# Performance work log

Measured on AMD Instinct MI355X. Metric: run time of the kernel, lower is better.

## Reference

```python
import jax, jax.numpy as jnp
import numpy as np

B, S, E, H, ROT, MAXP = 2, 1024, 2048, 16, 64, 2048
HD = E // H
EPS = 1e-12  # torch F.normalize default eps


def _sinusoidal_positions(num_pos, dim):
    # GPT-J create_sinusoidal_positions: concat(sin, cos) along feature dim
    inv_freq = 1.0 / (10000.0 ** (np.arange(0, dim, 2, dtype=np.float32) / dim))
    sinusoid = np.einsum("i,j->ij", np.arange(num_pos, dtype=np.float32), inv_freq)
    return jnp.asarray(np.concatenate([np.sin(sinusoid), np.cos(sinusoid)], axis=-1))


def _rotate_every_two(x):
    x1 = x[..., ::2]
    x2 = x[..., 1::2]
    return jnp.stack((-x2, x1), axis=-1).reshape(x.shape)


def _apply_rotary(t, sin, cos):
    # t: [B,S,H,rot]; sin/cos: [B,S,rot/2] -> repeat_interleave(2) -> [B,S,1,rot]
    sin = jnp.repeat(sin, 2, axis=-1)[:, :, None, :]
    cos = jnp.repeat(cos, 2, axis=-1)[:, :, None, :]
    return t * cos + _rotate_every_two(t) * sin


def setup_inputs() -> dict:
    key = jax.random.key(0)
    ks = jax.random.split(key, 5)
    hidden_states = jax.random.normal(ks[0], (B, S, E), dtype=jnp.float32)
    w_q = jax.random.normal(ks[1], (E, E), dtype=jnp.float32) * 0.02
    w_k = jax.random.normal(ks[2], (E, E), dtype=jnp.float32) * 0.02
    w_v = jax.random.normal(ks[3], (E, E), dtype=jnp.float32) * 0.02
    w_o = jax.random.normal(ks[4], (E, E), dtype=jnp.float32) * 0.02
    norm_const = 0.5 * jnp.ones((1, H, 1, 1), dtype=jnp.float32)
    attention_mask = jnp.zeros((B, 1, 1, S), dtype=jnp.float32)  # 0 = attend (HF additive mask)
    position_ids = jnp.tile(jnp.arange(S, dtype=jnp.int32)[None, :], (B, 1))
    return {"hidden_states": hidden_states, "w_q": w_q, "w_k": w_k, "w_v": w_v,
            "w_o": w_o, "norm_const": norm_const, "attention_mask": attention_mask,
            "position_ids": position_ids}


def reference(hidden_states, w_q, w_k, w_v, w_o, norm_const, attention_mask, position_ids):
    b, s, e = hidden_states.shape
    # projections (nn.Linear, no bias): y = x @ W.T
    q = (hidden_states @ w_q.T).reshape(b, s, H, HD)  # rotary layout [B,S,H,hd]
    k = (hidden_states @ w_k.T).reshape(b, s, H, HD)
    v = (hidden_states @ w_v.T).reshape(b, s, H, HD).transpose(0, 2, 1, 3)  # [B,H,S,hd]

    embed = _sinusoidal_positions(MAXP, ROT)          # [MAXP, ROT]
    sincos = embed[position_ids]                      # [B,S,ROT]
    sin, cos = jnp.split(sincos, 2, axis=-1)          # each [B,S,ROT/2]

    # partial rotary on first ROT dims
    q = jnp.concatenate([_apply_rotary(q[..., :ROT], sin, cos), q[..., ROT:]], axis=-1)
    k = jnp.concatenate([_apply_rotary(k[..., :ROT], sin, cos), k[..., ROT:]], axis=-1)
    q = q.transpose(0, 2, 1, 3)  # [B,H,S,hd]
    k = k.transpose(0, 2, 1, 3)

    causal = jnp.tril(jnp.ones((s, s), dtype=bool))[None, None]   # [1,1,S,S]
    mask0 = (attention_mask == 0)                                  # [B,1,1,S] bool

    # value rescale: per-query count of visible keys ** sigmoid(norm_const), clamped >= 1
    counts = jnp.sum(causal & mask0, axis=-1, keepdims=True).astype(jnp.float32)  # [B,1,S,1]
    denom = jnp.maximum(counts ** jax.nn.sigmoid(norm_const), 1.0)                # [B,H,S,1]
    v = v / denom

    # L2-normalize q/k (torch F.normalize: x / max(||x||, eps))
    q = q / jnp.maximum(jnp.linalg.norm(q, axis=-1, keepdims=True), EPS)
    k = k / jnp.maximum(jnp.linalg.norm(k, axis=-1, keepdims=True), EPS)

    mask_t = jnp.swapaxes(mask0, -1, -2)  # [B,1,S,1]
    q = q * mask_t
    k = k * mask_t
    v = v * mask_t

    attn_weights = jnp.einsum("bhqd,bhkd->bhqk", q, k)     # cosine similarities
    attn_weights = jnp.where(causal, attn_weights, 0.0)
    attn_output = jnp.einsum("bhqk,bhkd->bhqd", attn_weights, v)

    attn_output = attn_output.transpose(0, 2, 1, 3).reshape(b, s, e)
    return attn_output @ w_o.T
```

## Files before the change

kernel.cpp:

```cpp
#include <hip/hip_runtime.h>
#include <math.h>

#define B 2
#define S 1024
#define E 2048
#define H 16
#define HD 128
#define ROT 64
#define EPSN 1e-12f

using half8 = __attribute__((ext_vector_type(8))) _Float16;
using half4 = __attribute__((ext_vector_type(4))) _Float16;
using half2 = __attribute__((ext_vector_type(2))) _Float16;
using f32x4 = __attribute__((ext_vector_type(4))) float;

__device__ __forceinline__ void gl_lds16(const void* g, void* l) {
    __builtin_amdgcn_global_load_lds(
        (const __attribute__((address_space(1))) unsigned int*)g,
        (__attribute__((address_space(3))) unsigned int*)l, 16, 0, 0);
}

#define BARX()   asm volatile("s_barrier" ::: "memory")
#define VMW(n)   asm volatile("s_waitcnt vmcnt(" #n ")" ::: "memory")
#define SCHEDB() __builtin_amdgcn_sched_barrier(0)

__device__ __forceinline__ int ctIdx(int row, int col) {
    return row * 256 + (col & 3) + ((((col >> 2) ^ ((row >> 3) & 15)) & 63) << 2);
}

__global__ __launch_bounds__(256) void f2h5(const float* __restrict__ x0,
                                            const float* __restrict__ x1,
                                            const float* __restrict__ x2,
                                            const float* __restrict__ x3,
                                            const float* __restrict__ x4,
                                            _Float16* __restrict__ y0,
                                            _Float16* __restrict__ y1,
                                            _Float16* __restrict__ y2,
                                            _Float16* __restrict__ y3,
                                            _Float16* __restrict__ y4) {
    const float* xs[5] = {x0, x1, x2, x3, x4};
    _Float16*    ys[5] = {y0, y1, y2, y3, y4};
    const int t = blockIdx.y;
    const int i = blockIdx.x * 256 + threadIdx.x;
    float4 v = ((const float4*)xs[t])[i];
    half4 h;
    h[0] = (_Float16)v.x; h[1] = (_Float16)v.y;
    h[2] = (_Float16)v.z; h[3] = (_Float16)v.w;
    ((half4*)ys[t])[i] = h;
}

__global__ __launch_bounds__(1024) void countprep(const float* __restrict__ am,
                                                  float* __restrict__ cnt) {
    __shared__ float sc[1024];
    const int b = blockIdx.x, t = threadIdx.x;
    sc[t] = (am[b * S + t] == 0.f) ? 1.f : 0.f;
    __syncthreads();
    for (int off = 1; off < 1024; off <<= 1) {
        float u = (t >= off) ? sc[t - off] : 0.f;
        __syncthreads();
        sc[t] += u;
        __syncthreads();
    }
    cnt[b * S + t] = sc[t];
}

__global__ __launch_bounds__(512, 2) void gemm_qkv256(
        const _Float16* __restrict__ hs,
        const _Float16* __restrict__ wq,
        const _Float16* __restrict__ wk,
        const _Float16* __restrict__ wv,
        _Float16* __restrict__ qo,
        _Float16* __restrict__ ko,
        _Float16* __restrict__ kto,
        _Float16* __restrict__ vto,
        const float* __restrict__ am,
        const int*  __restrict__ pos,
        const float* __restrict__ nc,
        const float* __restrict__ cnt) {
    __shared__ uint4 L[8][1024];
    __shared__ float sclA[256], sclB[256];

    const int lid = (int)blockIdx.x;
    const int swz = (lid & 7) * 24 + (lid >> 3);
    const int z   = swz >> 6;
    const int gm  = (swz & 63) >> 3;
    const int gn  = swz & 7;
    const _Float16* Wp = (z == 0) ? wq : (z == 1) ? wk : wv;
    const int mBase = gm << 8;
    const int nBase = gn << 8;

    const int tid   = (int)threadIdx.x;
    const int lane  = tid & 63;
    const int w     = tid >> 6;
    const int l15   = lane & 15;
    const int lq    = lane >> 4;
    const int wm4   = (w >> 2) << 2;
    const int wn2   = (w & 3) << 1;
    const int wbase = tid & 448;

    const int bb  = mBase >> 10;
    const int sB0 = mBase & (S - 1);
    const int h0  = gn * 2;

    if (tid < 256) {
        const int sgx = sB0 + tid;
        float valid = (am[bb * S + sgx] == 0.f) ? 1.f : 0.f;
        if (z == 2) {
            float c  = cnt[bb * S + sgx];
            float g0 = 1.f / (1.f + expf(-nc[h0]));
            float g1 = 1.f / (1.f + expf(-nc[h0 + 1]));
            sclA[tid] = valid / fmaxf(powf(c, g0), 1.f);
            sclB[tid] = valid / fmaxf(powf(c, g1), 1.f);
        } else {
            sclA[tid] = valid;
        }
    }

    f32x4 acc[2][2][4][2];
#pragma unroll
    for (int X = 0; X < 2; ++X)
#pragma unroll
        for (int Y = 0; Y < 2; ++Y)
#pragma unroll
            for (int mt = 0; mt < 4; ++mt)
#pragma unroll
                for (int nt = 0; nt < 2; ++nt)
                    acc[X][Y][mt][nt] = (f32x4){0.f, 0.f, 0.f, 0.f};

    half8 afA[4][2], afB[4][2], wfA[2][2], wfB[2][2];

    auto stage = [&](int slot, const _Float16* src, int rowBase, int hf, int kt) {
#pragma unroll
        for (int j = 0; j < 2; ++j) {
            const int c  = (j << 9) + tid;
            const int rb = c >> 7;
            const int q  = (c >> 4) & 7;
            const int r  = c & 15;
            gl_lds16(&src[(size_t)(rowBase + hf * 128 + rb * 16 + r) * E +
                          kt * 64 + q * 8],
                     &L[slot][(j << 9) + wbase]);
        }
    };
    auto ldsA = [&](half8 (&dst)[4][2], int slot) {
#pragma unroll
        for (int mt = 0; mt < 4; ++mt)
#pragma unroll
            for (int ks = 0; ks < 2; ++ks)
                dst[mt][ks] = *(const half8*)&L[slot]
                    [(wm4 + mt) * 128 + (ks * 4 + lq) * 16 + l15];
    };
    auto ldsB = [&](half8 (&dst)[2][2], int slot) {
#pragma unroll
        for (int nt = 0; nt < 2; ++nt)
#pragma unroll
            for (int ks = 0; ks < 2; ++ks)
                dst[nt][ks] = *(const half8*)&L[slot]
                    [(wn2 + nt) * 128 + (ks * 4 + lq) * 16 + l15];
    };

#define MMAQ(X, Y, Af, Bf)                                                     \
    do {                                                                       \
        __builtin_amdgcn_s_setprio(1);                                         \
        _Pragma("unroll") for (int mt = 0; mt < 4; ++mt)                       \
            _Pragma("unroll") for (int nt = 0; nt < 2; ++nt)                   \
                _Pragma("unroll") for (int ks = 0; ks < 2; ++ks)               \
                    acc[X][Y][mt][nt] = __builtin_amdgcn_mfma_f32_16x16x32_f16(\
                        Af[mt][ks], Bf[nt][ks], acc[X][Y][mt][nt], 0, 0, 0);   \
        __builtin_amdgcn_s_setprio(0);                                         \
    } while (0)

    stage(0, hs, mBase, 0, 0);
    stage(4, Wp, nBase, 0, 0);
    stage(1, hs, mBase, 1, 0);
    stage(5, Wp, nBase, 1, 0);
    stage(2, hs, mBase, 0, 1);
    stage(7, Wp, nBase, 1, 1);
    stage(3, hs, mBase, 1, 1);
    VMW(6);
    BARX();
    ldsA(afA, 0);
    ldsB(wfA, 4);

    for (int j = 0; j < 16; ++j) {
        const int tB  = 2 * j + 1;
        const int tN0 = 2 * j + 2;
        const int tN1 = 2 * j + 3;
        const bool more = (j < 15);

        BARX();
        ldsB(wfB, 5);
        stage(6, Wp, nBase, 0, tB);
        SCHEDB();
        MMAQ(0, 0, afA, wfA);

        BARX();
        ldsA(afB, 1);
        if (more) stage(0, hs, mBase, 0, tN0);
        SCHEDB();
        MMAQ(0, 1, afA, wfB);

        BARX();
        if (more) stage(5, Wp, nBase, 1, tN0);
        SCHEDB();
        MMAQ(1, 1, afB, wfB);

        if (more) { VMW(4); } else { VMW(0); }
        BARX();
        ldsA(afA, 2);
        ldsB(wfB, 6);
        if (more) stage(1, hs, mBase, 1, tN0);
        SCHEDB();
        MMAQ(1, 0, afB, wfA);

        BARX();
        ldsB(wfA, 7);
        if (more) stage(4, Wp, nBase, 0, tN0);
        SCHEDB();
        MMAQ(0, 0, afA, wfB);

        BARX();
        ldsA(afB, 3);
        if (more) stage(2, hs, mBase, 0, tN1);
        SCHEDB();
        MMAQ(0, 1, afA, wfA);

        BARX();
        if (more) stage(7, Wp, nBase, 1, tN1);
        SCHEDB();
        MMAQ(1, 1, afB, wfA);

        VMW(4);
        BARX();
        ldsA(afA, 0);
        ldsB(wfA, 4);
        if (more) stage(3, hs, mBase, 1, tN1);
        SCHEDB();
        MMAQ(1, 0, afB, wfB);
    }

    BARX();
    _Float16* CtH = (_Float16*)&L[0][0];
#pragma unroll
    for (int X = 0; X < 2; ++X)
#pragma unroll
        for (int Y = 0; Y < 2; ++Y)
#pragma unroll
            for (int mt = 0; mt < 4; ++mt)
#pragma unroll
                for (int nt = 0; nt < 2; ++nt)
#pragma unroll
                    for (int r = 0; r < 4; ++r) {
                        int row = X * 128 + (w >> 2) * 64 + mt * 16 + lq * 4 + r;
                        int col = Y * 128 + (w & 3) * 32 + nt * 16 + l15;
                        float v = acc[X][Y][mt][nt][r];
                        if (z == 2) v *= (Y ? sclB[row] : sclA[row]);
                        CtH[ctIdx(row, col)] = (_Float16)v;
                    }
    __syncthreads();

    if (z < 2) {
        _Float16* rowOut = (z == 0) ? qo : ko;
        const int hh = lane >> 5;
        const int il = lane & 31;
        for (int rr = 0; rr < 32; ++rr) {
            int row = w * 32 + rr;
            int sg  = sB0 + row;
            float p = (float)pos[bb * S + sg];
            half4 x = *(const half4*)&CtH[ctIdx(row, hh * 128 + il * 4)];
            float v0 = x[0], v1 = x[1], v2 = x[2], v3 = x[3];
            if (il < 16) {
                float a0 = p * expf(-0.28782313662425574f * (float)(2 * il));
                float a1 = p * expf(-0.28782313662425574f * (float)(2 * il + 1));
                float s0, c0, s1, c1;
                sincosf(a0, &s0, &c0);
                sincosf(a1, &s1, &c1);
                float t0 = v0 * c0 - v1 * s0, t1 = v1 * c0 + v0 * s0;
                float t2 = v2 * c1 - v3 * s1, t3 = v3 * c1 + v2 * s1;
                v0 = t0; v1 = t1; v2 = t2; v3 = t3;
            }
            float ss = v0 * v0 + v1 * v1 + v2 * v2 + v3 * v3;
            ss += __shfl_xor(ss, 1);  ss += __shfl_xor(ss, 2);
            ss += __shfl_xor(ss, 4);  ss += __shfl_xor(ss, 8);
            ss += __shfl_xor(ss, 16);
            float scl = sclA[row] / fmaxf(sqrtf(ss), EPSN);
            half4 y;
            y[0] = (_Float16)(v0 * scl); y[1] = (_Float16)(v1 * scl);
            y[2] = (_Float16)(v2 * scl); y[3] = (_Float16)(v3 * scl);
            *(half4*)&rowOut[(((size_t)bb * H + h0 + hh) * S + sg) * HD +
                             il * 4] = y;
            if (z == 1)
                *(half4*)&CtH[ctIdx(row, hh * 128 + il * 4)] = y;
        }
    }
    if (z >= 1) {
        if (z == 1) __syncthreads();
        _Float16* To = (z == 1) ? kto : vto;
#pragma unroll
        for (int i = 0; i < 16; ++i) {
            int cch = tid + i * 512;
            int dr  = cch >> 5;
            int sc  = cch & 31;
            half8 hv;
#pragma unroll
            for (int jj = 0; jj < 8; ++jj)
                hv[jj] = CtH[ctIdx(sc * 8 + jj, dr)];
            *(half8*)&To[(((size_t)bb * H + h0 + (dr >> 7)) * HD + (dr & 127)) * S +
                         sB0 + sc * 8] = hv;
        }
    }
#undef MMAQ
}

__global__ __launch_bounds__(256) void gemm_out(const _Float16* __restrict__ A,
                                                const _Float16* __restrict__ Wp,
                                                float* __restrict__ C) {
    __shared__ uint4 As_l[2][512];
    __shared__ uint4 Ws_l[2][512];
    const int lid = (int)blockIdx.x;
    const int swz = (lid & 7) * 32 + (lid >> 3);
    const int gm  = swz >> 4;
    const int gn  = swz & 15;
    const int tid  = threadIdx.x;
    const int lane = tid & 63;
    const int w    = tid >> 6;
    const int wm   = (w >> 1) * 64;
    const int wn   = (w & 1) * 64;
    const int l15  = lane & 15;
    const int lq   = lane >> 4;
    const int r16  = lane & 15;
    const int kq4  = lane >> 4;
    const int mBase = gm * 128;
    const int nBase = gn * 128;

    f32x4 acc[4][4];
#pragma unroll
    for (int mt = 0; mt < 4; ++mt)
#pragma unroll
        for (int nt = 0; nt < 4; ++nt)
            acc[mt][nt] = (f32x4){0.f, 0.f, 0.f, 0.f};

    auto stage = [&](int bf, int k0) {
#pragma unroll
        for (int i = 0; i < 2; ++i) {
            int rb = w * 2 + i;
            gl_lds16(&A[(size_t)(mBase + rb * 16 + r16) * E + k0 + kq4 * 8],
                     &As_l[bf][rb * 64]);
            gl_lds16(&Wp[(size_t)(nBase + rb * 16 + r16) * E + k0 + kq4 * 8],
                     &Ws_l[bf][rb * 64]);
        }
    };

    stage(0, 0);
    const int nIter = E / 32;
    for (int it = 0; it < nIter; ++it) {
        __syncthreads();
        if (it + 1 < nIter) stage((it + 1) & 1, (it + 1) * 32);

        const int cur = it & 1;
        half8 af[4], wfr[4];
#pragma unroll
        for (int t = 0; t < 4; ++t) {
            int rbA = (wm >> 4) + t;
            int rbW = (wn >> 4) + t;
            af[t]  = *(const half8*)&As_l[cur][rbA * 64 + lq * 16 + l15];
            wfr[t] = *(const half8*)&Ws_l[cur][rbW * 64 + lq * 16 + l15];
        }
#pragma unroll
        for (int mt = 0; mt < 4; ++mt)
#pragma unroll
            for (int nt = 0; nt < 4; ++nt)
                acc[mt][nt] = __builtin_amdgcn_mfma_f32_16x16x32_f16(
                    af[mt], wfr[nt], acc[mt][nt], 0, 0, 0);
    }

#pragma unroll
    for (int mt = 0; mt < 4; ++mt)
#pragma unroll
        for (int nt = 0; nt < 4; ++nt)
#pragma unroll
            for (int r = 0; r < 4; ++r) {
                int row = mBase + wm + mt * 16 + lq * 4 + r;
                int col = nBase + wn + nt * 16 + l15;
                C[(size_t)row * E + col] = acc[mt][nt][r];
            }
}

__global__ __launch_bounds__(256) void kvouter(const _Float16* __restrict__ kt,
                                               const _Float16* __restrict__ vt,
                                               _Float16* __restrict__ ut) {
    __shared__ __align__(16) _Float16 SB[2 * 128 * 72];
    _Float16 (*Kt_s)[72] = (_Float16(*)[72])SB;
    _Float16 (*Vt_s)[72] = (_Float16(*)[72])(SB + 128 * 72);
    const int c  = blockIdx.x;
    const int bh = blockIdx.y;
    const int tid = threadIdx.x;
    const int lane = tid & 63, w = tid >> 6;
    const int l15 = lane & 15, lq = lane >> 4;
    const size_t ds_b = (size_t)bh * HD * S + (size_t)c * 64;

    uint4 pk[4], pv[4];
#pragma unroll
    for (int j = 0; j < 4; ++j) {
        int f = tid + j * 256;
        int d = f >> 3, c8 = f & 7;
        pk[j] = *(const uint4*)&kt[ds_b + (size_t)d * S + c8 * 8];
        pv[j] = *(const uint4*)&vt[ds_b + (size_t)d * S + c8 * 8];
    }
#pragma unroll
    for (int j = 0; j < 4; ++j) {
        int f = tid + j * 256;
        int d = f >> 3, c8 = f & 7;
        *(uint4*)&Kt_s[d][c8 * 8] = pk[j];
        *(uint4*)&Vt_s[d][c8 * 8] = pv[j];
    }
    __syncthreads();

    f32x4 acc[2][8];
#pragma unroll
    for (int mt = 0; mt < 2; ++mt)
#pragma unroll
        for (int nt = 0; nt < 8; ++nt)
            acc[mt][nt] = (f32x4){0.f, 0.f, 0.f, 0.f};

#pragma unroll
    for (int ks = 0; ks < 2; ++ks) {
        half8 af[2], wf[8];
#pragma unroll
        for (int mt = 0; mt < 2; ++mt)
            af[mt] = *(const half8*)&Kt_s[(w * 2 + mt) * 16 + l15][ks * 32 + lq * 8];
#pragma unroll
        for (int nt = 0; nt < 8; ++nt)
            wf[nt] = *(const half8*)&Vt_s[nt * 16 + l15][ks * 32 + lq * 8];
#pragma unroll
        for (int mt = 0; mt < 2; ++mt)
#pragma unroll
            for (int nt = 0; nt < 8; ++nt)
                acc[mt][nt] = __builtin_amdgcn_mfma_f32_16x16x32_f16(
                    af[mt], wf[nt], acc[mt][nt], 0, 0, 0);
    }
    __syncthreads();

    _Float16* Mb = SB;
#pragma unroll
    for (int mt = 0; mt < 2; ++mt)
#pragma unroll
        for (int nt = 0; nt < 8; ++nt)
#pragma unroll
            for (int r = 0; r < 4; ++r) {
                int dk = (w * 2 + mt) * 16 + lq * 4 + r;
                int flat = nt * 2048 + (dk >> 5) * 512 +
                           (l15 + ((dk >> 3) & 3) * 16) * 8 + (dk & 7);
                Mb[flat] = (_Float16)acc[mt][nt][r];
            }
    __syncthreads();

    const size_t ub = ((size_t)bh * 16 + c) << 14;
#pragma unroll
    for (int j = 0; j < 8; ++j) {
        int f = tid + j * 256;
        *(uint4*)&ut[ub + (size_t)f * 8] = *(const uint4*)&Mb[f * 8];
    }
}

__global__ __launch_bounds__(256) void prefix16(_Float16* __restrict__ u) {
    const int sl = blockIdx.x & 7;
    const int bh = blockIdx.x >> 3;
    const size_t base = (size_t)bh * 16 * 16384 + sl * 2048 + threadIdx.x * 8;
    float acc[8] = {0.f, 0.f, 0.f, 0.f, 0.f, 0.f, 0.f, 0.f};
    half8 nxt = *(const half8*)&u[base];
#pragma unroll
    for (int c = 0; c < 16; ++c) {
        half8 cur = nxt;
        if (c < 15) nxt = *(const half8*)&u[base + (size_t)(c + 1) * 16384];
        half8 outv;
#pragma unroll
        for (int i = 0; i < 8; ++i) outv[i] = (_Float16)acc[i];
        *(half8*)&u[base + (size_t)c * 16384] = outv;
#pragma unroll
        for (int i = 0; i < 8; ++i) acc[i] += (float)cur[i];
    }
}

__global__ __launch_bounds__(256) void attn_local(const _Float16* __restrict__ qh,
                                                  const _Float16* __restrict__ kh,
                                                  const _Float16* __restrict__ vt,
                                                  const _Float16* __restrict__ mt,
                                                  _Float16* __restrict__ o) {
    __shared__ _Float16 Ks[64][136];
    __shared__ _Float16 Vs[HD][72];
    __shared__ _Float16 Ps[64][72];
    __shared__ uint4 Ms[2048];

    const int qt = blockIdx.x;
    const int bh = blockIdx.y;
    const int b = bh >> 4, h = bh & 15;
    const int tid = threadIdx.x;
    const int lane = tid & 63;
    const int w = tid >> 6;
    const int l15 = lane & 15;
    const int lq = lane >> 4;
    const int qBase = qt * 64;
    const size_t sd_base = (size_t)bh * S * HD;

    half8 qf[4];
#pragma unroll
    for (int ks = 0; ks < 4; ++ks)
        qf[ks] = *(const half8*)&qh[sd_base + (size_t)(qBase + w * 16 + l15) * HD +
                                    ks * 32 + lq * 8];

    const _Float16* mtc = mt + (((size_t)bh * 16 + qt) << 14);
#pragma unroll
    for (int rr = 0; rr < 8; ++rr)
        gl_lds16(&mtc[(size_t)((rr * 4 + w) * 64 + lane) * 8],
                 &Ms[(rr * 4 + w) * 64]);

    uint4 pk[4], pv[4];
#pragma unroll
    for (int j = 0; j < 4; ++j) {
        int f = tid + j * 256;
        int rK = f >> 4, c8K = f & 15;
        int rV = f >> 3, c8V = f & 7;
        pk[j] = *(const uint4*)&kh[sd_base + (size_t)(qBase + rK) * HD + c8K * 8];
        pv[j] = *(const uint4*)&vt[sd_base + (size_t)rV * S + qBase + c8V * 8];
    }
#pragma unroll
    for (int j = 0; j < 4; ++j) {
        int f = tid + j * 256;
        int rK = f >> 4, c8K = f & 15;
        int rV = f >> 3, c8V = f & 7;
        *(uint4*)&Ks[rK][c8K * 8] = pk[j];
        *(uint4*)&Vs[rV][c8V * 8] = pv[j];
    }
    __syncthreads();

    f32x4 sacc[4];
#pragma unroll
    for (int nt = 0; nt < 4; ++nt)
        sacc[nt] = (f32x4){0.f, 0.f, 0.f, 0.f};
#pragma unroll
    for (int nt = 0; nt < 4; ++nt)
#pragma unroll
        for (int ks = 0; ks < 4; ++ks) {
            half8 kf = *(const half8*)&Ks[nt * 16 + l15][ks * 32 + lq * 8];
            sacc[nt] = __builtin_amdgcn_mfma_f32_16x16x32_f16(qf[ks], kf,
                                                              sacc[nt], 0, 0, 0);
        }

#pragma unroll
    for (int nt = 0; nt < 4; ++nt)
#pragma unroll
        for (int r = 0; r < 4; ++r) {
            int ql = w * 16 + lq * 4 + r;
            int kl = nt * 16 + l15;
            float sv = (kl <= ql) ? sacc[nt][r] : 0.f;
            Ps[ql][kl] = (_Float16)sv;
        }

    f32x4 oacc[8];
#pragma unroll
    for (int dt = 0; dt < 8; ++dt)
        oacc[dt] = (f32x4){0.f, 0.f, 0.f, 0.f};
#pragma unroll
    for (int dt = 0; dt < 8; ++dt)
#pragma unroll
        for (int km = 0; km < 4; ++km) {
            half8 mf = *(const half8*)&Ms[(dt * 4 + km) * 64 + lane];
            oacc[dt] = __builtin_amdgcn_mfma_f32_16x16x32_f16(qf[km], mf,
                                                              oacc[dt], 0, 0, 0);
        }
    __syncthreads();

    half8 pf[2];
    pf[0] = *(const half8*)&Ps[w * 16 + l15][lq * 8];
    pf[1] = *(const half8*)&Ps[w * 16 + l15][32 + lq * 8];
#pragma unroll
    for (int dt = 0; dt < 8; ++dt)
#pragma unroll
        for (int ks = 0; ks < 2; ++ks) {
            half8 vf = *(const half8*)&Vs[dt * 16 + l15][ks * 32 + lq * 8];
            oacc[dt] = __builtin_amdgcn_mfma_f32_16x16x32_f16(pf[ks], vf,
                                                              oacc[dt], 0, 0, 0);
        }

#pragma unroll
    for (int dt = 0; dt < 8; ++dt)
#pragma unroll
        for (int r = 0; r < 4; ++r)
            Ks[w * 16 + lq * 4 + r][dt * 16 + l15] = (_Float16)oacc[dt][r];
    __syncthreads();
#pragma unroll
    for (int j = 0; j < 4; ++j) {
        int f = tid + j * 256;
        int ql = f >> 4, c8 = f & 15;
        *(uint4*)&o[(size_t)(b * S + qBase + ql) * E + h * HD + c8 * 8] =
            *(const uint4*)&Ks[ql][c8 * 8];
    }
}

extern "C" void kernel_launch(void* const* d_in, const int* in_sizes, int n_in,
                              void* d_out, int out_size, void* d_ws, size_t ws_size,
                              hipStream_t stream) {
    (void)in_sizes; (void)n_in; (void)out_size; (void)ws_size;
    const float* hs = (const float*)d_in[0];
    const float* wq = (const float*)d_in[1];
    const float* wk = (const float*)d_in[2];
    const float* wv = (const float*)d_in[3];
    const float* wo = (const float*)d_in[4];
    const float* nc = (const float*)d_in[5];
    const float* am = (const float*)d_in[6];
    const int*  pos = (const int*)d_in[7];
    float* out = (float*)d_out;

    const size_t act = (size_t)B * S * E;
    _Float16* hsb = (_Float16*)d_ws;
    _Float16* wqb = hsb + act;
    _Float16* wkb = wqb + act;
    _Float16* wvb = wkb + act;
    _Float16* wob = wvb + act;
    _Float16* qhh = wob + act;
    _Float16* khh = qhh + act;
    _Float16* ktt = khh + act;
    _Float16* vtt = ktt + act;
    _Float16* abb = vtt + act;
    _Float16* utm = wqb;
    float*    cnt = (float*)abb;

    f2h5<<<dim3((int)(act / 4 / 256), 5), 256, 0, stream>>>(
        hs, wq, wk, wv, wo, hsb, wqb, wkb, wvb, wob);

    countprep<<<B, 1024, 0, stream>>>(am, cnt);

    gemm_qkv256<<<192, 512, 0, stream>>>(hsb, wqb, wkb, wvb,
                                         qhh, khh, ktt, vtt, am, pos, nc, cnt);

    kvouter<<<dim3(16, B * H), 256, 0, stream>>>(ktt, vtt, utm);
    prefix16<<<B * H * 8, 256, 0, stream>>>(utm);
    attn_local<<<dim3(16, B * H), 256, 0, stream>>>(qhh, khh, vtt, utm, abb);

    gemm_out<<<256, 256, 0, stream>>>(abb, wob, out);
}
```

Before: 357.9 us.

## Replace register double-buffered fragments with single-buffer lds load then barrier-wait per quadrant

The QKV projection main loop previously kept two sets of A/B register fragments (afA/afB, wfA/wfB) and prefetched the next LDS fragments while MFMAs ran, with sched_barriers ordering the steps. Now a single fragment set is loaded from LDS, followed by a barrier and an lgkmcnt(0) wait before each MFMA quadrant, with another barrier after it. This cuts register pressure and simplifies ordering. In exchange, LDS reads no longer overlap with MFMA work and the loop runs about twice as many barriers, which can add stalls. Some fragments are also reloaded that were previously reused from registers.

```diff
diff --git a/kernel.cpp b/kernel.cpp
--- a/kernel.cpp
+++ b/kernel.cpp
@@ -20,9 +20,9 @@
         (__attribute__((address_space(3))) unsigned int*)l, 16, 0, 0);
 }
 
-#define BARX()   asm volatile("s_barrier" ::: "memory")
-#define VMW(n)   asm volatile("s_waitcnt vmcnt(" #n ")" ::: "memory")
-#define SCHEDB() __builtin_amdgcn_sched_barrier(0)
+#define BARX()  asm volatile("s_barrier" ::: "memory")
+#define LGKM0() asm volatile("s_waitcnt lgkmcnt(0)" ::: "memory")
+#define VMW(n)  asm volatile("s_waitcnt vmcnt(" #n ")" ::: "memory")
 
 __device__ __forceinline__ int ctIdx(int row, int col) {
     return row * 256 + (col & 3) + ((((col >> 2) ^ ((row >> 3) & 15)) & 63) << 2);
@@ -127,7 +127,7 @@
                 for (int nt = 0; nt < 2; ++nt)
                     acc[X][Y][mt][nt] = (f32x4){0.f, 0.f, 0.f, 0.f};
 
-    half8 afA[4][2], afB[4][2], wfA[2][2], wfB[2][2];
+    half8 af[4][2], wf[2][2];
 
     auto stage = [&](int slot, const _Float16* src, int rowBase, int hf, int kt) {
 #pragma unroll
@@ -141,33 +141,34 @@
                      &L[slot][(j << 9) + wbase]);
         }
     };
-    auto ldsA = [&](half8 (&dst)[4][2], int slot) {
+    auto ldsA = [&](int db, int X) {
 #pragma unroll
         for (int mt = 0; mt < 4; ++mt)
 #pragma unroll
             for (int ks = 0; ks < 2; ++ks)
-                dst[mt][ks] = *(const half8*)&L[slot]
+                af[mt][ks] = *(const half8*)&L[db * 2 + X]
                     [(wm4 + mt) * 128 + (ks * 4 + lq) * 16 + l15];
     };
-    auto ldsB = [&](half8 (&dst)[2][2], int slot) {
+    auto ldsB = [&](int db, int Y) {
 #pragma unroll
         for (int nt = 0; nt < 2; ++nt)
 #pragma unroll
             for (int ks = 0; ks < 2; ++ks)
-                dst[nt][ks] = *(const half8*)&L[slot]
+                wf[nt][ks] = *(const half8*)&L[4 + db * 2 + Y]
                     [(wn2 + nt) * 128 + (ks * 4 + lq) * 16 + l15];
     };
-
-#define MMAQ(X, Y, Af, Bf)                                                     \
-    do {                                                                       \
-        __builtin_amdgcn_s_setprio(1);                                         \
-        _Pragma("unroll") for (int mt = 0; mt < 4; ++mt)                       \
-            _Pragma("unroll") for (int nt = 0; nt < 2; ++nt)                   \
-                _Pragma("unroll") for (int ks = 0; ks < 2; ++ks)               \
-                    acc[X][Y][mt][nt] = __builtin_amdgcn_mfma_f32_16x16x32_f16(\
-                        Af[mt][ks], Bf[nt][ks], acc[X][Y][mt][nt], 0, 0, 0);   \
-        __builtin_amdgcn_s_setprio(0);                                         \
-    } while (0)
+    auto mma = [&](int X, int Y) {
+        __builtin_amdgcn_s_setprio(1);
+#pragma unroll
+        for (int mt = 0; mt < 4; ++mt)
+#pragma unroll
+            for (int nt = 0; nt < 2; ++nt)
+#pragma unroll
+                for (int ks = 0; ks < 2; ++ks)
+                    acc[X][Y][mt][nt] = __builtin_amdgcn_mfma_f32_16x16x32_f16(
+                        af[mt][ks], wf[nt][ks], acc[X][Y][mt][nt], 0, 0, 0);
+        __builtin_amdgcn_s_setprio(0);
+    };
 
     stage(0, hs, mBase, 0, 0);
     stage(4, Wp, nBase, 0, 0);
@@ -178,8 +179,6 @@
     stage(3, hs, mBase, 1, 1);
     VMW(6);
     BARX();
-    ldsA(afA, 0);
-    ldsB(wfA, 4);
 
     for (int j = 0; j < 16; ++j) {
         const int tB  = 2 * j + 1;
@@ -187,57 +186,58 @@
         const int tN1 = 2 * j + 3;
         const bool more = (j < 15);
 
-        BARX();
-        ldsB(wfB, 5);
+        ldsA(0, 0); ldsB(0, 0);
         stage(6, Wp, nBase, 0, tB);
-        SCHEDB();
-        MMAQ(0, 0, afA, wfA);
-
-        BARX();
-        ldsA(afB, 1);
+        BARX(); LGKM0();
+        mma(0, 0);
+        BARX();
+
+        ldsB(0, 1);
         if (more) stage(0, hs, mBase, 0, tN0);
-        SCHEDB();
-        MMAQ(0, 1, afA, wfB);
-
-        BARX();
+        BARX(); LGKM0();
+        mma(0, 1);
+        BARX();
+
+        ldsA(0, 1);
         if (more) stage(5, Wp, nBase, 1, tN0);
-        SCHEDB();
-        MMAQ(1, 1, afB, wfB);
-
-        if (more) { VMW(4); } else { VMW(0); }
-        BARX();
-        ldsA(afA, 2);
-        ldsB(wfB, 6);
-        if (more) stage(1, hs, mBase, 1, tN0);
-        SCHEDB();
-        MMAQ(1, 0, afB, wfA);
-
-        BARX();
-        ldsB(wfA, 7);
+        BARX(); LGKM0();
+        mma(1, 1);
+        BARX();
+
+        ldsB(0, 0);
+        if (more) { stage(1, hs, mBase, 1, tN0); VMW(4); }
+        else      { VMW(0); }
+        BARX(); LGKM0();
+        mma(1, 0);
+        BARX();
+
+        ldsA(1, 0); ldsB(1, 0);
         if (more) stage(4, Wp, nBase, 0, tN0);
-        SCHEDB();
-        MMAQ(0, 0, afA, wfB);
-
-        BARX();
-        ldsA(afB, 3);
+        BARX(); LGKM0();
+        mma(0, 0);
+        BARX();
+
+        ldsB(1, 1);
         if (more) stage(2, hs, mBase, 0, tN1);
-        SCHEDB();
-        MMAQ(0, 1, afA, wfA);
-
-        BARX();
+        BARX(); LGKM0();
+        mma(0, 1);
+        BARX();
+
+        ldsA(1, 1);
         if (more) stage(7, Wp, nBase, 1, tN1);
-        SCHEDB();
-        MMAQ(1, 1, afB, wfA);
-
+        BARX(); LGKM0();
+        mma(1, 1);
+        BARX();
+
+        ldsB(1, 0);
+        if (more) stage(3, hs, mBase, 1, tN1);
         VMW(4);
-        BARX();
-        ldsA(afA, 0);
-        ldsB(wfA, 4);
-        if (more) stage(3, hs, mBase, 1, tN1);
-        SCHEDB();
-        MMAQ(1, 0, afB, wfB);
-    }
-
+        BARX(); LGKM0();
+        mma(1, 0);
+        BARX();
+    }
+
+    VMW(0);
     BARX();
     _Float16* CtH = (_Float16*)&L[0][0];
 #pragma unroll
@@ -308,7 +308,6 @@
                          sB0 + sc * 8] = hv;
         }
     }
-#undef MMAQ
 }
 
 __global__ __launch_bounds__(256) void gemm_out(const _Float16* __restrict__ A,
```

New measurement: 325.0 us. 1.1x faster.
